# Optimization experiments

Measured on AMD Instinct MI355X. Metric: run time of the kernel, lower is better.

Reference implementation:

```python
import jax, jax.numpy as jnp
import numpy as np


def setup_inputs() -> dict:
    key = jax.random.key(0)
    k1, k2 = jax.random.split(key)
    b, d = 8192, 256
    x = jax.random.normal(k1, (b, d), dtype=jnp.float32)
    dc = jax.random.uniform(k2, (b, d), dtype=jnp.float32)
    dc_param = jnp.array([0.05], dtype=jnp.float32)
    return {"x": x, "dc": dc, "dc_param": dc_param}


def reference(x, dc, dc_param):
    # Faithful to torch: sim[i,j] = 1 / mean_k[(1-p)*(x[i,k]-x[j,k])^2
    #                                        + p*exp(1-dc[i,k])*exp(1-dc[j,k])]
    # Expanded to GEMMs to avoid the O(b^2*d) broadcast intermediate:
    #   mean_k (x_i - x_j)^2 = (|x_i|^2 + |x_j|^2 - 2 x_i.x_j) / d
    #   mean_k e_i[k] e_j[k] = (e_i . e_j) / d,  e = exp(1 - dc)
    b, d = x.shape
    p = dc_param[0]
    sq = jnp.sum(x * x, axis=1)                      # (b,)
    msd = (sq[:, None] + sq[None, :] - 2.0 * (x @ x.T)) / d  # (b,b)
    e = jnp.exp(1.0 - dc)                            # (b,d)
    mker = (e @ e.T) / d                             # (b,b)
    sim = 1.0 / ((1.0 - p) * msd + p * mker)
    eye = jnp.eye(b, dtype=x.dtype)
    return sim * (1.0 - eye) + eye
```

## Files before the change

### kernel.cpp

```cpp
#include <hip/hip_runtime.h>
#include <hip/hip_bf16.h>

typedef __attribute__((ext_vector_type(8))) __bf16 bf16x8;
typedef __attribute__((ext_vector_type(4))) float  f32x4;

constexpr int NROW = 8192;
constexpr int DDIM = 256;
constexpr int KDIM = 512;
constexpr int BM = 256, BN = 128, BK = 32;
constexpr int NT = KDIM / BK;
constexpr int ABYTES = BM * BK * 2;
constexpr int BBYTES = BN * BK * 2;
constexpr int BUFBYTES = ABYTES + BBYTES;

__device__ __forceinline__ void gload_lds16(const void* g, void* l) {
  __builtin_amdgcn_global_load_lds(
      (const __attribute__((address_space(1))) void*)g,
      (__attribute__((address_space(3))) void*)l, 16, 0, 0);
}

__global__ __launch_bounds__(256) void prep_kernel(
    const float* __restrict__ x, const float* __restrict__ dc,
    const float* __restrict__ pparm,
    __hip_bfloat16* __restrict__ P, float* __restrict__ s)
{
  const int row = blockIdx.x;
  const int t   = threadIdx.x;
  const float xv = x[(size_t)row * DDIM + t];
  const float ev = __expf(1.0f - dc[(size_t)row * DDIM + t]);
  P[(size_t)row * KDIM + t]        = __float2bfloat16(xv);
  P[(size_t)row * KDIM + DDIM + t] = __float2bfloat16(ev);

  float v = xv * xv;
  #pragma unroll
  for (int off = 32; off > 0; off >>= 1) v += __shfl_down(v, off, 64);
  __shared__ float red[4];
  const int lane = t & 63, wid = t >> 6;
  if (lane == 0) red[wid] = v;
  __syncthreads();
  if (t == 0) {
    const float p = pparm[0];
    s[row] = (1.0f - p) * (1.0f / (float)DDIM) * (red[0] + red[1] + red[2] + red[3]);
  }
}

__global__ void __launch_bounds__(512, 4) adj_gemm(
    const __hip_bfloat16* __restrict__ P, const float* __restrict__ s,
    const float* __restrict__ pparm, float* __restrict__ out)
{
  __shared__ __align__(16) char lds[65536];

  const float p  = pparm[0];
  const float cx = -2.0f * (1.0f - p) / (float)DDIM;
  const float ce = p / (float)DDIM;
  const float midscale = cx / ce;

  const int orig = blockIdx.x;
  const int bi = orig >> 6;
  const int bj = orig & 63;
  const int rowBase = bi * BM;
  const int colBase = bj * BN;

  const int tid  = threadIdx.x;
  const int lane = tid & 63;
  const int wid  = tid >> 6;
  const int wmrow = (wid >> 1) * 64;
  const int wnrow = (wid & 1) * 64;
  const int frow = lane & 15;
  const int kq   = lane >> 4;

  const int cb = (kq * 16) ^ ((frow & 3) << 4);

  const int rA0  = tid >> 2;
  const int gcol = ((tid & 3) * 16) ^ ((rA0 & 3) << 4);
  const char* Pc = (const char*)P;
  const char* gA0 = Pc + (size_t)(rowBase + rA0)       * (KDIM * 2) + gcol;
  const char* gA1 = Pc + (size_t)(rowBase + 128 + rA0) * (KDIM * 2) + gcol;
  const char* gB  = Pc + (size_t)(colBase + rA0)       * (KDIM * 2) + gcol;
  const int dA0 = tid * 16, dA1 = 8192 + tid * 16, dB = ABYTES + tid * 16;

#define STAGE(kk) do {                                   \
    char* _b = lds + ((kk) & 1) * BUFBYTES;              \
    const int _ko = (kk) * (BK * 2);                     \
    gload_lds16(gA0 + _ko, _b + dA0);                    \
    gload_lds16(gA1 + _ko, _b + dA1);                    \
    gload_lds16(gB  + _ko, _b + dB);                     \
  } while (0)

  STAGE(0);
  asm volatile("s_waitcnt vmcnt(0)" ::: "memory");
  asm volatile("s_barrier" ::: "memory");

  f32x4 acc[4][4];
  #pragma unroll
  for (int m = 0; m < 4; ++m)
    #pragma unroll
    for (int n = 0; n < 4; ++n)
      acc[m][n] = (f32x4){0.f, 0.f, 0.f, 0.f};

  #pragma unroll
  for (int t = 0; t < NT; ++t) {
    const char* buf  = lds + (t & 1) * BUFBYTES;
    const char* bufB = buf + ABYTES;

    if (t < NT - 1) STAGE(t + 1);

    bf16x8 a[4], b[4];
    #pragma unroll
    for (int i = 0; i < 4; ++i)
      a[i] = *(const bf16x8*)(buf + (wmrow + i * 16 + frow) * 64 + cb);
    #pragma unroll
    for (int j = 0; j < 4; ++j)
      b[j] = *(const bf16x8*)(bufB + (wnrow + j * 16 + frow) * 64 + cb);

    #pragma unroll
    for (int i = 0; i < 4; ++i)
      #pragma unroll
      for (int j = 0; j < 4; ++j)
        acc[i][j] = __builtin_amdgcn_mfma_f32_16x16x32_bf16(a[i], b[j], acc[i][j], 0, 0, 0);

    if (t == DDIM / BK - 1) {
      #pragma unroll
      for (int m = 0; m < 4; ++m)
        #pragma unroll
        for (int n = 0; n < 4; ++n)
          acc[m][n] *= midscale;
    }

    if (t < NT - 1) {
      asm volatile("s_waitcnt vmcnt(0)" ::: "memory");
      asm volatile("s_barrier" ::: "memory");
    }
  }

  float* ldsf = (float*)lds;
  const int rq = lane >> 4;

  #pragma unroll
  for (int h = 0; h < 2; ++h) {
    __syncthreads();
    #pragma unroll
    for (int j = 0; j < 2; ++j) {
      const int n = 2 * h + j;
      const int gcol_o = colBase + wnrow + n * 16 + frow;
      const float scol = s[gcol_o];
      #pragma unroll
      for (int m = 0; m < 4; ++m) {
        #pragma unroll
        for (int r = 0; r < 4; ++r) {
          const int R = wmrow + m * 16 + rq * 4 + r;
          const int grow = rowBase + R;
          const float denom = s[grow] + scol + ce * acc[m][n][r];
          const float val = (grow == gcol_o) ? 1.0f : __builtin_amdgcn_rcpf(denom);
          const int cc = (j * 16 + frow) ^ (((R >> 2) & 1) << 4);
          ldsf[(wid & 1) * 8192 + R * 32 + cc] = val;
        }
      }
    }
    __syncthreads();
    #pragma unroll
    for (int i = 0; i < 8; ++i) {
      const int idx = i * 512 + tid;
      const int R   = idx >> 4;
      const int q   = idx & 15;
      const int st  = q >> 3;
      const int qq  = q & 7;
      const int ccs = (qq * 4) ^ (((R >> 2) & 1) << 4);
      const f32x4 v = *(const f32x4*)&ldsf[st * 8192 + R * 32 + ccs];
      const int col = colBase + st * 64 + h * 32 + qq * 4;
      *(f32x4*)&out[(size_t)(rowBase + R) * NROW + col] = v;
    }
  }
}

extern "C" void kernel_launch(void* const* d_in, const int* in_sizes, int n_in,
                              void* d_out, int out_size, void* d_ws, size_t ws_size,
                              hipStream_t stream) {
  const float* x  = (const float*)d_in[0];
  const float* dc = (const float*)d_in[1];
  const float* pp = (const float*)d_in[2];
  float* out = (float*)d_out;

  __hip_bfloat16* P = (__hip_bfloat16*)d_ws;
  float* s = (float*)((char*)d_ws + (size_t)NROW * KDIM * 2);

  prep_kernel<<<NROW, 256, 0, stream>>>(x, dc, pp, P, s);
  adj_gemm<<<(NROW / BM) * (NROW / BN), 512, 0, stream>>>(P, s, pp, out);
}
```

Measured before the change: 119.4 us.

## Exploit symmetry: compute upper-triangular tiles and write transposed mirror

The similarity matrix is symmetric, so the GEMM now launches only the tiles on or above the block diagonal and maps each block index to its triangular tile coordinates. Off-diagonal tiles also write their transpose through a rotated LDS staging buffer. This roughly halves the MFMA work and operand loads. In exchange, the direct output stores are now per-element and strided rather than vectorised, and the mirror tiles carry extra LDS traffic and barriers.

```diff
diff --git a/kernel.cpp b/kernel.cpp
--- a/kernel.cpp
+++ b/kernel.cpp
@@ -1,5 +1,6 @@
 #include <hip/hip_runtime.h>
 #include <hip/hip_bf16.h>
+#include <math.h>
 
 typedef __attribute__((ext_vector_type(8))) __bf16 bf16x8;
 typedef __attribute__((ext_vector_type(4))) float  f32x4;
@@ -12,6 +13,7 @@
 constexpr int ABYTES = BM * BK * 2;
 constexpr int BBYTES = BN * BK * 2;
 constexpr int BUFBYTES = ABYTES + BBYTES;
+constexpr int NBLK = 1056;
 
 __device__ __forceinline__ void gload_lds16(const void* g, void* l) {
   __builtin_amdgcn_global_load_lds(
@@ -56,10 +58,13 @@
   const float midscale = cx / ce;
 
   const int orig = blockIdx.x;
-  const int bi = orig >> 6;
-  const int bj = orig & 63;
+  int bi = (int)((65.0f - sqrtf(65.0f * 65.0f - 4.0f * (float)orig)) * 0.5f);
+  while (bi > 0 && bi * (65 - bi) > orig) --bi;
+  while ((bi + 1) * (65 - (bi + 1)) <= orig) ++bi;
+  const int bj = 2 * bi + (orig - bi * (65 - bi));
   const int rowBase = bi * BM;
   const int colBase = bj * BN;
+  const bool mirror = (bj >= 2 * bi + 2);
 
   const int tid  = threadIdx.x;
   const int lane = tid & 63;
@@ -68,15 +73,16 @@
   const int wnrow = (wid & 1) * 64;
   const int frow = lane & 15;
   const int kq   = lane >> 4;
+  const int rq   = lane >> 4;
 
   const int cb = (kq * 16) ^ ((frow & 3) << 4);
 
   const int rA0  = tid >> 2;
-  const int gcol = ((tid & 3) * 16) ^ ((rA0 & 3) << 4);
+  const int gcw  = ((tid & 3) * 16) ^ ((rA0 & 3) << 4);
   const char* Pc = (const char*)P;
-  const char* gA0 = Pc + (size_t)(rowBase + rA0)       * (KDIM * 2) + gcol;
-  const char* gA1 = Pc + (size_t)(rowBase + 128 + rA0) * (KDIM * 2) + gcol;
-  const char* gB  = Pc + (size_t)(colBase + rA0)       * (KDIM * 2) + gcol;
+  const char* gA0 = Pc + (size_t)(rowBase + rA0)       * (KDIM * 2) + gcw;
+  const char* gA1 = Pc + (size_t)(rowBase + 128 + rA0) * (KDIM * 2) + gcw;
+  const char* gB  = Pc + (size_t)(colBase + rA0)       * (KDIM * 2) + gcw;
   const int dA0 = tid * 16, dA1 = 8192 + tid * 16, dB = ABYTES + tid * 16;
 
 #define STAGE(kk) do {                                   \
@@ -134,16 +140,18 @@
   }
 
   float* ldsf = (float*)lds;
-  const int rq = lane >> 4;
+  const int st_w = wid & 1;
+
+  if (mirror) __syncthreads();
 
   #pragma unroll
   for (int h = 0; h < 2; ++h) {
-    __syncthreads();
+    if (mirror && h) __syncthreads();
     #pragma unroll
     for (int j = 0; j < 2; ++j) {
       const int n = 2 * h + j;
-      const int gcol_o = colBase + wnrow + n * 16 + frow;
-      const float scol = s[gcol_o];
+      const int gcol = colBase + wnrow + n * 16 + frow;
+      const float scol = s[gcol];
       #pragma unroll
       for (int m = 0; m < 4; ++m) {
         #pragma unroll
@@ -151,24 +159,30 @@
           const int R = wmrow + m * 16 + rq * 4 + r;
           const int grow = rowBase + R;
           const float denom = s[grow] + scol + ce * acc[m][n][r];
-          const float val = (grow == gcol_o) ? 1.0f : __builtin_amdgcn_rcpf(denom);
-          const int cc = (j * 16 + frow) ^ (((R >> 2) & 1) << 4);
-          ldsf[(wid & 1) * 8192 + R * 32 + cc] = val;
+          const float val = (grow == gcol) ? 1.0f : __builtin_amdgcn_rcpf(denom);
+          out[(size_t)grow * NROW + gcol] = val;
+          if (mirror) {
+            const int c32 = j * 16 + frow;
+            const int cc = (c32 + (R >> 2) + 8 * (R & 3)) & 31;
+            ldsf[st_w * 8192 + R * 32 + cc] = val;
+          }
         }
       }
     }
-    __syncthreads();
-    #pragma unroll
-    for (int i = 0; i < 8; ++i) {
-      const int idx = i * 512 + tid;
-      const int R   = idx >> 4;
-      const int q   = idx & 15;
-      const int st  = q >> 3;
-      const int qq  = q & 7;
-      const int ccs = (qq * 4) ^ (((R >> 2) & 1) << 4);
-      const f32x4 v = *(const f32x4*)&ldsf[st * 8192 + R * 32 + ccs];
-      const int col = colBase + st * 64 + h * 32 + qq * 4;
-      *(f32x4*)&out[(size_t)(rowBase + R) * NROW + col] = v;
+    if (mirror) {
+      __syncthreads();
+      #pragma unroll
+      for (int i = 0; i < 8; ++i) {
+        const int cl  = i * 8 + wid;
+        const int st  = cl >> 5;
+        const int c32 = cl & 31;
+        const int gTrow = colBase + st * 64 + 32 * h + c32;
+        f32x4 v;
+        #pragma unroll
+        for (int r = 0; r < 4; ++r)
+          v[r] = ldsf[st * 8192 + (4 * lane + r) * 32 + ((c32 + lane + 8 * r) & 31)];
+        *(f32x4*)&out[(size_t)gTrow * NROW + rowBase + 4 * lane] = v;
+      }
     }
   }
 }
@@ -185,5 +199,5 @@
   float* s = (float*)((char*)d_ws + (size_t)NROW * KDIM * 2);
 
   prep_kernel<<<NROW, 256, 0, stream>>>(x, dc, pp, P, s);
-  adj_gemm<<<(NROW / BM) * (NROW / BN), 512, 0, stream>>>(P, s, pp, out);
-}
+  adj_gemm<<<NBLK, 512, 0, stream>>>(P, s, pp, out);
+}
```

New measurement: 132.9 us. 1.11x slower.
